# Performance work log

Hardware: AMD Instinct MI355X
Metric: run time of the kernel (lower is better)

The kernel has to match this reference:

```python
import jax, jax.numpy as jnp
import numpy as np

N = 50000      # nodes
E = 500000     # edges
G = 8          # graphs in batch
IN = 128       # in_dim
HID = 64       # hidden_dim_graph == hidden_dim1
H = 2          # num_heads
C = 2          # n_classes
SLOPE = 0.2    # DGL GATConv leaky_relu negative slope


def setup_inputs() -> dict:
    key = jax.random.key(0)
    ks = jax.random.split(key, 16)
    s = lambda k, sh, fan: (jax.random.normal(k, sh, jnp.float32) / np.float32(np.sqrt(fan)))
    return {
        "h_n": jax.random.normal(ks[0], (N, IN), jnp.float32),
        "src": jax.random.randint(ks[1], (E,), 0, N),
        "dst": jax.random.randint(ks[2], (E,), 0, N),
        "graph_ids": jnp.sort(jax.random.randint(ks[3], (N,), 0, G)),
        # GATConv layer 1: fc [IN, H*HID], attn vectors [H, HID]
        "W_fc1": s(ks[4], (IN, H * HID), IN),
        "attn_l1": s(ks[5], (H, HID), HID),
        "attn_r1": s(ks[6], (H, HID), HID),
        # GATConv layer 2: fc [HID, H*HID]
        "W_fc2": s(ks[7], (HID, H * HID), HID),
        "attn_l2": s(ks[8], (H, HID), HID),
        "attn_r2": s(ks[9], (H, HID), HID),
        # gate nn: Linear(HID, 1)
        "w_gate": s(ks[10], (HID, 1), HID),
        "b_gate": jnp.zeros((1,), jnp.float32),
        # classifier MLP
        "W_c1": s(ks[11], (HID, HID), HID),
        "b_c1": jnp.zeros((HID,), jnp.float32),
        "W_c2": s(ks[12], (HID, C), HID),
        "b_c2": jnp.zeros((C,), jnp.float32),
    }


def _gat_conv(h, src, dst, W_fc, attn_l, attn_r):
    # h: [N, D_in] -> out: [N, H, HID]
    feat = (h @ W_fc).reshape(N, H, HID)
    el = (feat * attn_l).sum(-1)                 # [N, H]
    er = (feat * attn_r).sum(-1)                 # [N, H]
    e = jax.nn.leaky_relu(el[src] + er[dst], SLOPE)   # [E, H]
    # edge softmax over incoming edges per destination node
    m = jax.ops.segment_max(e, dst, num_segments=N)   # [N, H]
    ex = jnp.exp(e - m[dst])                     # [E, H]
    den = jax.ops.segment_sum(ex, dst, num_segments=N)
    alpha = ex / jnp.where(den == 0, 1.0, den)[dst]
    # message passing: sum_e alpha_e * feat[src_e]
    return jax.ops.segment_sum(alpha[:, :, None] * feat[src], dst, num_segments=N)


def _segment_softmax(x, ids, num_segments):
    m = jax.ops.segment_max(x, ids, num_segments=num_segments)
    ex = jnp.exp(x - m[ids])
    den = jax.ops.segment_sum(ex, ids, num_segments=num_segments)
    return ex / jnp.where(den == 0, 1.0, den)[ids]


def reference(h_n, src, dst, graph_ids, W_fc1, attn_l1, attn_r1, W_fc2, attn_l2,
              attn_r2, w_gate, b_gate, W_c1, b_c1, W_c2, b_c2):
    h = jax.nn.relu(_gat_conv(h_n, src, dst, W_fc1, attn_l1, attn_r1)).mean(axis=1)
    h = jax.nn.relu(_gat_conv(h, src, dst, W_fc2, attn_l2, attn_r2)).mean(axis=1)
    # global attention pooling (gate MLP + per-graph softmax + weighted sum)
    gate = (h @ w_gate + b_gate)[:, 0]                 # [N]
    a = _segment_softmax(gate, graph_ids, G)[:, None]  # [N, 1]
    hg = jax.ops.segment_sum(a * h, graph_ids, num_segments=G)  # [G, HID]
    # classifier head (dropout is identity in eval mode)
    a2 = hg @ W_c1 + b_c1
    a3 = a2 @ W_c2 + b_c2
    return (jax.nn.sigmoid(a3), a, hg)
```

## Files before the change

### kernel.cpp

```cpp
#include <hip/hip_runtime.h>
#include <hip/hip_bf16.h>

#define NN 50000
#define EE 500000
#define GG 8
#define INDIM 128
#define HID 64
#define NH 2
#define PB 32
#define TMM 64
#define CAP 32
#define NBF ((NN + TMM - 1) / TMM)
#define EPB ((EE + NBF - 1) / NBF)

typedef __bf16 bf16x4 __attribute__((ext_vector_type(4)));
typedef __bf16 bf16x8 __attribute__((ext_vector_type(8)));
typedef float  f32x4  __attribute__((ext_vector_type(4)));

__device__ inline unsigned short f2bf(float f) {
    unsigned int u = __float_as_uint(f);
    unsigned int r = (u + 0x7FFFu + ((u >> 16) & 1u)) >> 16;
    return (unsigned short)r;
}
__device__ inline unsigned int pack_bf16x2(float lo, float hi) {
    return (unsigned int)f2bf(lo) | ((unsigned int)f2bf(hi) << 16);
}
__device__ inline unsigned int encf(float f) {
    unsigned int u = __float_as_uint(f);
    return (u & 0x80000000u) ? ~u : (u | 0x80000000u);
}
__device__ inline float decf(unsigned int e) {
    unsigned int u = (e & 0x80000000u) ? (e & 0x7FFFFFFFu) : ~e;
    return __uint_as_float(u);
}
__device__ inline int lower_bound_g(const int* __restrict__ gids, int target, int N) {
    int lo = 0, hi = N;
    while (lo < hi) { int mid = (lo + hi) >> 1; if (gids[mid] < target) lo = mid + 1; else hi = mid; }
    return lo;
}

__global__ __launch_bounds__(256) void prep_kernel(
        const float* __restrict__ W1, const float* __restrict__ W2,
        unsigned short* __restrict__ Wf1, unsigned short* __restrict__ Wf2,
        unsigned int* __restrict__ zero_base) {
    int idx = blockIdx.x * 256 + threadIdx.x;
    const int ZN = GG + GG + GG * 64 + NN;
    if (idx < ZN) zero_base[idx] = 0u;
    if (idx < 128 * 128) {
        int c = idx >> 7, r = idx & 127;
        int ks = r >> 5, g = (r >> 3) & 3, e = r & 7;
        int k = ks * 32 + (e < 4 ? g * 4 + e : 16 + g * 4 + (e - 4));
        Wf1[idx] = f2bf(W1[k * 128 + c]);
    }
    if (idx < 128 * 64) {
        int c = idx >> 6, r = idx & 63;
        int ks = r >> 5, g = (r >> 3) & 3, e = r & 7;
        int k = ks * 32 + (e < 4 ? g * 4 + e : 16 + g * 4 + (e - 4));
        Wf2[idx] = f2bf(W2[k * 128 + c]);
    }
}

template <int K>
__device__ __forceinline__ void fc_mfma_body(
        int bid, const float* __restrict__ X,
        const unsigned short* __restrict__ Wf,
        const float* __restrict__ al, const float* __restrict__ ar,
        unsigned int* __restrict__ featb, float* __restrict__ el,
        float* __restrict__ er, int N) {
    __shared__ __align__(16) char smem[16384];
    char* Xb = smem;
    char* Dt = smem;

    constexpr int K2 = K * 2;
    constexpr int K4 = K / 4;
    constexpr int k4sh = (K == 128) ? 5 : 4;
    constexpr int nks = K / 32;

    int t = threadIdx.x;
    int n0 = bid * TMM;

    for (int i = t; i < TMM * K4; i += 256) {
        int row = i >> k4sh, c4 = i & (K4 - 1);
        int gr = n0 + row;
        float4 v = make_float4(0.f, 0.f, 0.f, 0.f);
        if (gr < N) v = *(const float4*)&X[(size_t)gr * K + (c4 << 2)];
        int slot = c4 ^ (row & 15);
        *(uint2*)(Xb + row * K2 + slot * 8) =
            make_uint2(pack_bf16x2(v.x, v.y), pack_bf16x2(v.z, v.w));
    }
    __syncthreads();

    int wv = t >> 6, l = t & 63;
    int lr = l & 15, g = l >> 4;

    bf16x8 bfr[nks][2];
#pragma unroll
    for (int ks = 0; ks < nks; ks++)
#pragma unroll
        for (int cb = 0; cb < 2; cb++) {
            int c = wv * 32 + cb * 16 + lr;
            bfr[ks][cb] = *(const bf16x8*)(Wf + (((size_t)c * nks + ks) * 4 + g) * 8);
        }

    f32x4 acc[4][2];
#pragma unroll
    for (int rb = 0; rb < 4; rb++)
#pragma unroll
        for (int cb = 0; cb < 2; cb++) acc[rb][cb] = (f32x4){0.f, 0.f, 0.f, 0.f};

#pragma unroll
    for (int ks = 0; ks < nks; ks++) {
        bf16x8 af[4];
#pragma unroll
        for (int rb = 0; rb < 4; rb++) {
            int r = rb * 16 + lr;
            const char* base = Xb + r * K2;
            int s0 = (ks * 8 + g) ^ (r & 15);
            int s1 = (ks * 8 + g + 4) ^ (r & 15);
            bf16x4 a0 = *(const bf16x4*)(base + s0 * 8);
            bf16x4 a1 = *(const bf16x4*)(base + s1 * 8);
            af[rb] = __builtin_shufflevector(a0, a1, 0, 1, 2, 3, 4, 5, 6, 7);
        }
#pragma unroll
        for (int rb = 0; rb < 4; rb++)
#pragma unroll
            for (int cb = 0; cb < 2; cb++)
                acc[rb][cb] = __builtin_amdgcn_mfma_f32_16x16x32_bf16(
                    af[rb], bfr[ks][cb], acc[rb][cb], 0, 0, 0);
    }
    __syncthreads();

#pragma unroll
    for (int rb = 0; rb < 4; rb++)
#pragma unroll
        for (int cb = 0; cb < 2; cb++)
#pragma unroll
            for (int j = 0; j < 4; j++) {
                int row = rb * 16 + 4 * g + j;
                int col = wv * 32 + cb * 16 + lr;
                int byte = (col * 2) ^ ((row & 7) << 4);
                *(unsigned short*)(Dt + row * 256 + byte) = f2bf(acc[rb][cb][j]);
            }
    __syncthreads();

    for (int i = t; i < TMM * 16; i += 256) {
        int row = i >> 4, s16 = i & 15;
        uint4 v = *(const uint4*)(Dt + row * 256 + ((s16 * 16) ^ ((row & 7) << 4)));
        int gr = n0 + row;
        if (gr < N) *(uint4*)&featb[(size_t)gr * 64 + s16 * 4] = v;
    }

    {
        int r = t >> 2, p = t & 3;
        int h = p >> 1;
        const float* alh = al + h * 64 + (p & 1) * 32;
        const float* arh = ar + h * 64 + (p & 1) * 32;
        float pl = 0.f, pr = 0.f;
#pragma unroll
        for (int ii = 0; ii < 4; ii++) {
            int s16 = p * 4 + ii;
            uint4 v = *(const uint4*)(Dt + r * 256 + ((s16 * 16) ^ ((r & 7) << 4)));
            unsigned int uu[4] = {v.x, v.y, v.z, v.w};
#pragma unroll
            for (int q = 0; q < 4; q++) {
                float flo = __uint_as_float(uu[q] << 16);
                float fhi = __uint_as_float(uu[q] & 0xFFFF0000u);
                int cb = ii * 8 + q * 2;
                pl += flo * alh[cb] + fhi * alh[cb + 1];
                pr += flo * arh[cb] + fhi * arh[cb + 1];
            }
        }
        pl += __shfl_xor(pl, 1, 64);
        pr += __shfl_xor(pr, 1, 64);
        int gr = n0 + r;
        if ((p & 1) == 0 && gr < N) {
            el[gr * 2 + h] = pl;
            er[gr * 2 + h] = pr;
        }
    }
}

__global__ __launch_bounds__(256) void build_fc1_kernel(
        const int* __restrict__ src, const int* __restrict__ dst,
        int* __restrict__ cnt, unsigned short* __restrict__ esrc,
        const float* __restrict__ X, const unsigned short* __restrict__ Wf,
        const float* __restrict__ al, const float* __restrict__ ar,
        unsigned int* __restrict__ featb, float* __restrict__ el,
        float* __restrict__ er) {
    int bid = blockIdx.x;
    int t = threadIdx.x;
    int eb = bid * EPB;
    int eend = eb + EPB;
    if (eend > EE) eend = EE;
    int dv[3], sv[3], pv[3];
    bool vv[3];
#pragma unroll
    for (int j = 0; j < 3; j++) {
        int e = eb + t + j * 256;
        vv[j] = e < eend;
        int es = vv[j] ? e : eb;
        dv[j] = dst[es];
        sv[j] = src[es];
    }
#pragma unroll
    for (int j = 0; j < 3; j++)
        if (vv[j]) pv[j] = atomicAdd(&cnt[dv[j]], 1);
#pragma unroll
    for (int j = 0; j < 3; j++)
        if (vv[j] && pv[j] < CAP)
            esrc[(size_t)dv[j] * CAP + pv[j]] = (unsigned short)sv[j];

    fc_mfma_body<128>(bid, X, Wf, al, ar, featb, el, er, NN);
}

__global__ __launch_bounds__(256) void fc_attn_kernel(
        const float* __restrict__ X, const unsigned short* __restrict__ Wf,
        const float* __restrict__ al, const float* __restrict__ ar,
        unsigned int* __restrict__ featb, float* __restrict__ el,
        float* __restrict__ er, int N) {
    fc_mfma_body<64>(blockIdx.x, X, Wf, al, ar, featb, el, er, N);
}

__global__ void gat_agg_kernel(const unsigned int* __restrict__ featb,
                               const float* __restrict__ el,
                               const float* __restrict__ er, const int* __restrict__ cnt,
                               const unsigned short* __restrict__ esrc,
                               float* __restrict__ hout,
                               const float* __restrict__ wg, const float* __restrict__ bg,
                               float* __restrict__ gatev, int doGate) {
    int wid = threadIdx.x >> 6;
    int lane = threadIdx.x & 63;
    int n = blockIdx.x * 4 + wid;
    if (n >= NN) return;
    int deg = cnt[n];
    deg = deg > CAP ? CAP : deg;
    int q = lane >> 4;
    int l4 = lane & 15;
    float a8[8];
#pragma unroll
    for (int i = 0; i < 8; i++) a8[i] = 0.f;

    if (deg > 0) {
        float2 erv = ((const float2*)er)[n];
        bool v = lane < deg;
        int s = (int)esrc[(size_t)n * CAP + (v ? lane : 0)];
        float2 elv = ((const float2*)el)[s];
        float e0 = elv.x + erv.x; e0 = e0 > 0.f ? e0 : 0.2f * e0;
        float e1 = elv.y + erv.y; e1 = e1 > 0.f ? e1 : 0.2f * e1;
        float x0 = v ? __expf(e0) : 0.f;
        float x1 = v ? __expf(e1) : 0.f;
        float d0 = x0, d1 = x1;
        for (int off = 32; off; off >>= 1) {
            d0 += __shfl_xor(d0, off, 64);
            d1 += __shfl_xor(d1, off, 64);
        }
        float a0 = x0 / d0, a1 = x1 / d1;
        int headHi = (l4 >= 8);
        for (int e = 0; e < deg; e += 4) {
            int myE = e + q;
            bool ve = myE < deg;
            int pick = ve ? myE : e;
            int se = __shfl(s, pick, 64);
            float av0 = __shfl(a0, pick, 64);
            float av1 = __shfl(a1, pick, 64);
            float a = headHi ? av1 : av0;
            if (!ve) a = 0.f;
            uint4 fv = *(const uint4*)&featb[(size_t)se * 64 + l4 * 4];
            a8[0] += a * __uint_as_float(fv.x << 16);
            a8[1] += a * __uint_as_float(fv.x & 0xFFFF0000u);
            a8[2] += a * __uint_as_float(fv.y << 16);
            a8[3] += a * __uint_as_float(fv.y & 0xFFFF0000u);
            a8[4] += a * __uint_as_float(fv.z << 16);
            a8[5] += a * __uint_as_float(fv.z & 0xFFFF0000u);
            a8[6] += a * __uint_as_float(fv.w << 16);
            a8[7] += a * __uint_as_float(fv.w & 0xFFFF0000u);
        }
    }

#pragma unroll
    for (int i = 0; i < 8; i++) {
        a8[i] += __shfl_xor(a8[i], 16, 64);
        a8[i] += __shfl_xor(a8[i], 32, 64);
        a8[i] = fmaxf(a8[i], 0.f);
    }
    float m8[8];
#pragma unroll
    for (int i = 0; i < 8; i++) m8[i] = 0.5f * (a8[i] + __shfl_xor(a8[i], 8, 64));
    if (lane < 8) {
        float4 w0 = make_float4(m8[0], m8[1], m8[2], m8[3]);
        float4 w1 = make_float4(m8[4], m8[5], m8[6], m8[7]);
        *(float4*)&hout[(size_t)n * 64 + 8 * lane] = w0;
        *(float4*)&hout[(size_t)n * 64 + 8 * lane + 4] = w1;
    }

    if (doGate) {
        float val = 0.f;
        if (lane < 8) {
#pragma unroll
            for (int i = 0; i < 8; i++) val += m8[i] * wg[8 * lane + i];
        }
        val += __shfl_xor(val, 1, 64);
        val += __shfl_xor(val, 2, 64);
        val += __shfl_xor(val, 4, 64);
        if (lane == 0) gatev[n] = val + bg[0];
    }
}

__global__ void pool_max_kernel(const float* __restrict__ gatev, const int* __restrict__ gids,
                                unsigned int* __restrict__ gmEnc) {
    int g = blockIdx.x / PB, b = blockIdx.x % PB;
    __shared__ int sb[2];
    int t = threadIdx.x;
    if (t == 0) { sb[0] = lower_bound_g(gids, g, NN); sb[1] = lower_bound_g(gids, g + 1, NN); }
    __syncthreads();
    int lo = sb[0], len = sb[1] - lo;
    int s = lo + (int)((long long)b * len / PB);
    int e = lo + (int)((long long)(b + 1) * len / PB);
    float m = -3.4e38f;
    for (int n = s + t; n < e; n += 256) m = fmaxf(m, gatev[n]);
    __shared__ float red[4];
    int w = t >> 6, lane = t & 63;
    for (int off = 32; off; off >>= 1) m = fmaxf(m, __shfl_down(m, off, 64));
    if (lane == 0) red[w] = m;
    __syncthreads();
    if (t == 0) {
        m = fmaxf(fmaxf(red[0], red[1]), fmaxf(red[2], red[3]));
        atomicMax(&gmEnc[g], encf(m));
    }
}

__global__ void pool_expacc_kernel(const float* __restrict__ h2, const float* __restrict__ gatev,
                                   const int* __restrict__ gids,
                                   const unsigned int* __restrict__ gmEnc,
                                   float* __restrict__ out_a, float* __restrict__ gsum,
                                   float* __restrict__ hgacc) {
    int g = blockIdx.x / PB, b = blockIdx.x % PB;
    __shared__ int sb[2];
    int t = threadIdx.x;
    if (t == 0) { sb[0] = lower_bound_g(gids, g, NN); sb[1] = lower_bound_g(gids, g + 1, NN); }
    __syncthreads();
    int lo = sb[0], len = sb[1] - lo;
    int s = lo + (int)((long long)b * len / PB);
    int e = lo + (int)((long long)(b + 1) * len / PB);
    float m = decf(gmEnc[g]);
    int sub = t >> 6, c = t & 63;
    float acc = 0.f, esum = 0.f;
    for (int n = s + sub; n < e; n += 4) {
        float ev = __expf(gatev[n] - m);
        if (c == 0) out_a[n] = ev;
        esum += ev;
        acc += ev * h2[(size_t)n * 64 + c];
    }
    __shared__ float sh[4][64];
    sh[sub][c] = acc;
    __syncthreads();
    if (sub == 0) atomicAdd(&hgacc[g * 64 + c], sh[0][c] + sh[1][c] + sh[2][c] + sh[3][c]);
    if (c == 0) atomicAdd(&gsum[g], esum);
}

__global__ __launch_bounds__(512) void epilogue_kernel(
        const float* __restrict__ hgacc, const float* __restrict__ gsum,
        const float* __restrict__ Wc1, const float* __restrict__ bc1,
        const float* __restrict__ Wc2, const float* __restrict__ bc2,
        const int* __restrict__ gids, float* __restrict__ out,
        float* __restrict__ out_a, float* __restrict__ out_hg) {
    int t = threadIdx.x;
    if (blockIdx.x != 0) {
        int n = (blockIdx.x - 1) * 512 + t;
        if (n < NN) {
            float sv = gsum[gids[n]];
            out_a[n] *= (sv > 0.f) ? 1.f / sv : 0.f;
        }
        return;
    }
    __shared__ float hgs[GG * 64];
    __shared__ float a2s[GG * 64];
    int g = t >> 6, c = t & 63;
    float sv = gsum[g];
    float inv = (sv > 0.f) ? 1.f / sv : 0.f;
    float hval = hgacc[t] * inv;
    hgs[t] = hval;
    out_hg[t] = hval;
    __syncthreads();
    float acc = bc1[c];
    for (int k = 0; k < 64; k++) acc += hgs[g * 64 + k] * Wc1[k * 64 + c];
    a2s[g * 64 + c] = acc;
    __syncthreads();
    if (t < GG * 2) {
        int gg = t >> 1, j = t & 1;
        float a3 = bc2[j];
        for (int k = 0; k < 64; k++) a3 += a2s[gg * 64 + k] * Wc2[k * 2 + j];
        out[t] = 1.f / (1.f + expf(-a3));
    }
}

extern "C" void kernel_launch(void* const* d_in, const int* in_sizes, int n_in,
                              void* d_out, int out_size, void* d_ws, size_t ws_size,
                              hipStream_t stream) {
    const float* h_n  = (const float*)d_in[0];
    const int*   src  = (const int*)d_in[1];
    const int*   dst  = (const int*)d_in[2];
    const int*   gids = (const int*)d_in[3];
    const float* Wfc1 = (const float*)d_in[4];
    const float* al1  = (const float*)d_in[5];
    const float* ar1  = (const float*)d_in[6];
    const float* Wfc2 = (const float*)d_in[7];
    const float* al2  = (const float*)d_in[8];
    const float* ar2  = (const float*)d_in[9];
    const float* wg   = (const float*)d_in[10];
    const float* bg   = (const float*)d_in[11];
    const float* Wc1  = (const float*)d_in[12];
    const float* bc1  = (const float*)d_in[13];
    const float* Wc2  = (const float*)d_in[14];
    const float* bc2  = (const float*)d_in[15];
    float* out = (float*)d_out;

    float* ws     = (float*)d_ws;
    unsigned int* featb = (unsigned int*)ws;
    float* el     = ws + (size_t)NN * 64;
    float* er     = el + NN * 2;
    float* hbuf   = er + NN * 2;
    float* gatev  = hbuf + (size_t)NN * 64;
    unsigned int* gmEnc = (unsigned int*)(gatev + NN);
    float* gsum   = (float*)(gmEnc + GG);
    float* hgacc  = gsum + GG;
    int*   cnt    = (int*)(hgacc + GG * 64);
    unsigned short* esrc = (unsigned short*)(cnt + NN);
    unsigned short* Wf1  = esrc + (size_t)NN * CAP;
    unsigned short* Wf2  = Wf1 + 128 * 128;

    const int ZN = GG + GG + GG * 64 + NN;
    prep_kernel<<<(ZN + 255) / 256, 256, 0, stream>>>(Wfc1, Wfc2, Wf1, Wf2, gmEnc);

    build_fc1_kernel<<<NBF, 256, 0, stream>>>(src, dst, cnt, esrc,
                                              h_n, Wf1, al1, ar1, featb, el, er);
    gat_agg_kernel<<<(NN + 3) / 4, 256, 0, stream>>>(featb, el, er, cnt, esrc, hbuf,
                                                     wg, bg, gatev, 0);

    fc_attn_kernel<<<NBF, 256, 0, stream>>>(hbuf, Wf2, al2, ar2,
                                            featb, el, er, NN);
    gat_agg_kernel<<<(NN + 3) / 4, 256, 0, stream>>>(featb, el, er, cnt, esrc, hbuf,
                                                     wg, bg, gatev, 1);

    pool_max_kernel<<<GG * PB, 256, 0, stream>>>(gatev, gids, gmEnc);
    pool_expacc_kernel<<<GG * PB, 256, 0, stream>>>(hbuf, gatev, gids, gmEnc,
                                                    out + GG * 2, gsum, hgacc);

    int nb = 1 + (NN + 511) / 512;
    epilogue_kernel<<<nb, 512, 0, stream>>>(hgacc, gsum, Wc1, bc1, Wc2, bc2, gids,
                                            out, out + GG * 2, out + GG * 2 + NN);
}
```

Before: 262.9 us.

## Halve FC row tile, overlap X loads with edge scatter, add occupancy hint

The node tile for the fused FC/attention kernels shrinks from 64 to 32 rows. That doubles the block count, halves shared memory per block, and lowers edges per block to at most 512. The X tile is now loaded into registers before the edge-binning atomics run and written to LDS afterwards, so global-load latency overlaps with the CSR build. Launch bounds request 4 blocks per SM to raise occupancy. In exchange, the weight fragments are reloaded per block twice as often and each block has less MFMA work.

```diff
diff --git a/kernel.cpp b/kernel.cpp
--- a/kernel.cpp
+++ b/kernel.cpp
@@ -8,7 +8,7 @@
 #define HID 64
 #define NH 2
 #define PB 32
-#define TMM 64
+#define TMM 32
 #define CAP 32
 #define NBF ((NN + TMM - 1) / TMM)
 #define EPB ((EE + NBF - 1) / NBF)
@@ -60,14 +60,16 @@
     }
 }
 
-template <int K>
+template <int K, bool SC>
 __device__ __forceinline__ void fc_mfma_body(
         int bid, const float* __restrict__ X,
         const unsigned short* __restrict__ Wf,
         const float* __restrict__ al, const float* __restrict__ ar,
         unsigned int* __restrict__ featb, float* __restrict__ el,
-        float* __restrict__ er, int N) {
-    __shared__ __align__(16) char smem[16384];
+        float* __restrict__ er, int N,
+        const int* __restrict__ src, const int* __restrict__ dst,
+        int* __restrict__ cnt, unsigned short* __restrict__ esrc) {
+    __shared__ __align__(16) char smem[8192];
     char* Xb = smem;
     char* Dt = smem;
 
@@ -75,19 +77,51 @@
     constexpr int K4 = K / 4;
     constexpr int k4sh = (K == 128) ? 5 : 4;
     constexpr int nks = K / 32;
+    constexpr int XIT = TMM * K4 / 256;
 
     int t = threadIdx.x;
     int n0 = bid * TMM;
 
-    for (int i = t; i < TMM * K4; i += 256) {
+    float4 xv[XIT];
+    int xrow[XIT], xslot[XIT];
+#pragma unroll
+    for (int u = 0; u < XIT; u++) {
+        int i = t + u * 256;
         int row = i >> k4sh, c4 = i & (K4 - 1);
         int gr = n0 + row;
-        float4 v = make_float4(0.f, 0.f, 0.f, 0.f);
-        if (gr < N) v = *(const float4*)&X[(size_t)gr * K + (c4 << 2)];
-        int slot = c4 ^ (row & 15);
-        *(uint2*)(Xb + row * K2 + slot * 8) =
-            make_uint2(pack_bf16x2(v.x, v.y), pack_bf16x2(v.z, v.w));
-    }
+        xv[u] = make_float4(0.f, 0.f, 0.f, 0.f);
+        if (gr < N) xv[u] = *(const float4*)&X[(size_t)gr * K + (c4 << 2)];
+        xrow[u] = row;
+        xslot[u] = c4 ^ (row & 15);
+    }
+
+    if (SC) {
+        int eb = bid * EPB;
+        int eend = eb + EPB;
+        if (eend > EE) eend = EE;
+        int dv[2], sv[2], pv[2];
+        bool vv[2];
+#pragma unroll
+        for (int j = 0; j < 2; j++) {
+            int e = eb + t + j * 256;
+            vv[j] = e < eend;
+            int es = vv[j] ? e : eb;
+            dv[j] = dst[es];
+            sv[j] = src[es];
+        }
+#pragma unroll
+        for (int j = 0; j < 2; j++)
+            if (vv[j]) pv[j] = atomicAdd(&cnt[dv[j]], 1);
+#pragma unroll
+        for (int j = 0; j < 2; j++)
+            if (vv[j] && pv[j] < CAP)
+                esrc[(size_t)dv[j] * CAP + pv[j]] = (unsigned short)sv[j];
+    }
+
+#pragma unroll
+    for (int u = 0; u < XIT; u++)
+        *(uint2*)(Xb + xrow[u] * K2 + xslot[u] * 8) =
+            make_uint2(pack_bf16x2(xv[u].x, xv[u].y), pack_bf16x2(xv[u].z, xv[u].w));
     __syncthreads();
 
     int wv = t >> 6, l = t & 63;
@@ -102,17 +136,17 @@
             bfr[ks][cb] = *(const bf16x8*)(Wf + (((size_t)c * nks + ks) * 4 + g) * 8);
         }
 
-    f32x4 acc[4][2];
-#pragma unroll
-    for (int rb = 0; rb < 4; rb++)
+    f32x4 acc[2][2];
+#pragma unroll
+    for (int rb = 0; rb < 2; rb++)
 #pragma unroll
         for (int cb = 0; cb < 2; cb++) acc[rb][cb] = (f32x4){0.f, 0.f, 0.f, 0.f};
 
 #pragma unroll
     for (int ks = 0; ks < nks; ks++) {
-        bf16x8 af[4];
-#pragma unroll
-        for (int rb = 0; rb < 4; rb++) {
+        bf16x8 af[2];
+#pragma unroll
+        for (int rb = 0; rb < 2; rb++) {
             int r = rb * 16 + lr;
             const char* base = Xb + r * K2;
             int s0 = (ks * 8 + g) ^ (r & 15);
@@ -122,7 +156,7 @@
             af[rb] = __builtin_shufflevector(a0, a1, 0, 1, 2, 3, 4, 5, 6, 7);
         }
 #pragma unroll
-        for (int rb = 0; rb < 4; rb++)
+        for (int rb = 0; rb < 2; rb++)
 #pragma unroll
             for (int cb = 0; cb < 2; cb++)
                 acc[rb][cb] = __builtin_amdgcn_mfma_f32_16x16x32_bf16(
@@ -131,7 +165,7 @@
     __syncthreads();
 
 #pragma unroll
-    for (int rb = 0; rb < 4; rb++)
+    for (int rb = 0; rb < 2; rb++)
 #pragma unroll
         for (int cb = 0; cb < 2; cb++)
 #pragma unroll
@@ -143,7 +177,9 @@
             }
     __syncthreads();
 
-    for (int i = t; i < TMM * 16; i += 256) {
+#pragma unroll
+    for (int u = 0; u < 2; u++) {
+        int i = t + u * 256;
         int row = i >> 4, s16 = i & 15;
         uint4 v = *(const uint4*)(Dt + row * 256 + ((s16 * 16) ^ ((row & 7) << 4)));
         int gr = n0 + row;
@@ -151,14 +187,14 @@
     }
 
     {
-        int r = t >> 2, p = t & 3;
-        int h = p >> 1;
-        const float* alh = al + h * 64 + (p & 1) * 32;
-        const float* arh = ar + h * 64 + (p & 1) * 32;
+        int r = t >> 3, p = t & 7;
+        int h = p >> 2;
+        const float* alh = al + h * 64 + (p & 3) * 16;
+        const float* arh = ar + h * 64 + (p & 3) * 16;
         float pl = 0.f, pr = 0.f;
 #pragma unroll
-        for (int ii = 0; ii < 4; ii++) {
-            int s16 = p * 4 + ii;
+        for (int ii = 0; ii < 2; ii++) {
+            int s16 = (p << 1) + ii;
             uint4 v = *(const uint4*)(Dt + r * 256 + ((s16 * 16) ^ ((r & 7) << 4)));
             unsigned int uu[4] = {v.x, v.y, v.z, v.w};
 #pragma unroll
@@ -172,53 +208,34 @@
         }
         pl += __shfl_xor(pl, 1, 64);
         pr += __shfl_xor(pr, 1, 64);
+        pl += __shfl_xor(pl, 2, 64);
+        pr += __shfl_xor(pr, 2, 64);
         int gr = n0 + r;
-        if ((p & 1) == 0 && gr < N) {
+        if ((p & 3) == 0 && gr < N) {
             el[gr * 2 + h] = pl;
             er[gr * 2 + h] = pr;
         }
     }
 }
 
-__global__ __launch_bounds__(256) void build_fc1_kernel(
+__global__ __launch_bounds__(256, 4) void build_fc1_kernel(
         const int* __restrict__ src, const int* __restrict__ dst,
         int* __restrict__ cnt, unsigned short* __restrict__ esrc,
         const float* __restrict__ X, const unsigned short* __restrict__ Wf,
         const float* __restrict__ al, const float* __restrict__ ar,
         unsigned int* __restrict__ featb, float* __restrict__ el,
         float* __restrict__ er) {
-    int bid = blockIdx.x;
-    int t = threadIdx.x;
-    int eb = bid * EPB;
-    int eend = eb + EPB;
-    if (eend > EE) eend = EE;
-    int dv[3], sv[3], pv[3];
-    bool vv[3];
-#pragma unroll
-    for (int j = 0; j < 3; j++) {
-        int e = eb + t + j * 256;
-        vv[j] = e < eend;
-        int es = vv[j] ? e : eb;
-        dv[j] = dst[es];
-        sv[j] = src[es];
-    }
-#pragma unroll
-    for (int j = 0; j < 3; j++)
-        if (vv[j]) pv[j] = atomicAdd(&cnt[dv[j]], 1);
-#pragma unroll
-    for (int j = 0; j < 3; j++)
-        if (vv[j] && pv[j] < CAP)
-            esrc[(size_t)dv[j] * CAP + pv[j]] = (unsigned short)sv[j];
-
-    fc_mfma_body<128>(bid, X, Wf, al, ar, featb, el, er, NN);
-}
-
-__global__ __launch_bounds__(256) void fc_attn_kernel(
+    fc_mfma_body<128, true>(blockIdx.x, X, Wf, al, ar, featb, el, er, NN,
+                            src, dst, cnt, esrc);
+}
+
+__global__ __launch_bounds__(256, 4) void fc_attn_kernel(
         const float* __restrict__ X, const unsigned short* __restrict__ Wf,
         const float* __restrict__ al, const float* __restrict__ ar,
         unsigned int* __restrict__ featb, float* __restrict__ el,
         float* __restrict__ er, int N) {
-    fc_mfma_body<64>(blockIdx.x, X, Wf, al, ar, featb, el, er, N);
+    fc_mfma_body<64, false>(blockIdx.x, X, Wf, al, ar, featb, el, er, N,
+                            nullptr, nullptr, nullptr, nullptr);
 }
 
 __global__ void gat_agg_kernel(const unsigned int* __restrict__ featb,
```

New measurement: 252.2 us. 4.1% less time.
